# Optimization experiments

Hardware: AMD Instinct MI355X
Metric: run time of the kernel (lower is better)

Reference implementation:

```python
import jax, jax.numpy as jnp
import numpy as np
import math

B, S, T, D, H = 4, 1024, 1024, 512, 8
EPS = 1e-5

def setup_inputs() -> dict:
    key = jax.random.key(0)
    ks = iter(jax.random.split(key, 40))
    w = lambda *shp: jax.random.normal(next(ks), shp, jnp.float32) * 0.02
    inp = {
        'x': jax.random.normal(next(ks), (B, S, D), jnp.float32),
        'encod_out': jax.random.normal(next(ks), (B, T, D), jnp.float32),
    }
    for p in ('sa', 'ca'):
        inp[p + '_wq'] = w(H, D, D); inp[p + '_bq'] = w(H, D)
        inp[p + '_wk'] = w(H, D, D); inp[p + '_bk'] = w(H, D)
        inp[p + '_wv'] = w(H, D, D); inp[p + '_bv'] = w(H, D)
        inp[p + '_wo'] = w(H, D, D); inp[p + '_bo'] = w(H, D)
        inp[p + '_wf'] = w(H * D, D); inp[p + '_bf'] = w(D)
    for i in (1, 2, 3):
        inp[f'ln{i}_g'] = jnp.ones((D,), jnp.float32)
        inp[f'ln{i}_b'] = jnp.zeros((D,), jnp.float32)
    inp['fc1_w'] = w(D, 4 * D); inp['fc1_b'] = w(4 * D)
    inp['fc2_w'] = w(4 * D, D); inp['fc2_b'] = w(D)
    return inp

def _ln(x, g, b):
    m = jnp.mean(x, -1, keepdims=True)
    v = jnp.mean((x - m) ** 2, -1, keepdims=True)
    return (x - m) / jnp.sqrt(v + EPS) * g + b

def _mha(xq, xkv, wq, bq, wk, bk, wv, bv, wo, bo, wf, bf, mask):
    # per-head FULL-width projections, stacked on head axis h
    Q = jnp.einsum('bsd,hdf->bhsf', xq, wq) + bq[None, :, None, :]
    K = jnp.einsum('btd,hdf->bhtf', xkv, wk) + bk[None, :, None, :]
    V = jnp.einsum('btd,hdf->bhtf', xkv, wv) + bv[None, :, None, :]
    scores = jnp.einsum('bhsf,bhtf->bhst', Q, K) / math.sqrt(Q.shape[-1])
    if mask is not None:
        scores = jnp.where(mask == 0, -jnp.inf, scores)
    A = jax.nn.softmax(scores, axis=-1)
    O = jnp.einsum('bhst,bhtf->bhsf', A, V)
    O = jnp.einsum('bhsf,hfg->bhsg', O, wo) + bo[None, :, None, :]  # per-head out_linear
    cat = O.transpose(0, 2, 1, 3).reshape(O.shape[0], O.shape[2], -1)  # [B,S,H*D]
    return cat @ wf + bf

def reference(x, encod_out,
              sa_wq, sa_bq, sa_wk, sa_bk, sa_wv, sa_bv, sa_wo, sa_bo, sa_wf, sa_bf,
              ca_wq, ca_bq, ca_wk, ca_bk, ca_wv, ca_bv, ca_wo, ca_bo, ca_wf, ca_bf,
              ln1_g, ln1_b, ln2_g, ln2_b, ln3_g, ln3_b,
              fc1_w, fc1_b, fc2_w, fc2_b):
    s = x.shape[1]
    mask = jnp.tril(jnp.ones((s, s), x.dtype))
    h = _mha(x, x, sa_wq, sa_bq, sa_wk, sa_bk, sa_wv, sa_bv, sa_wo, sa_bo, sa_wf, sa_bf, mask)
    x1 = _ln(h + x, ln1_g, ln1_b)
    h = _mha(x1, encod_out, ca_wq, ca_bq, ca_wk, ca_bk, ca_wv, ca_bv, ca_wo, ca_bo, ca_wf, ca_bf, None)
    x2 = _ln(h + x1, ln2_g, ln2_b)
    ff = jax.nn.relu(x2 @ fc1_w + fc1_b) @ fc2_w + fc2_b
    return _ln(ff + x2, ln3_g, ln3_b)
```

## Files before the change

kernel.cpp:

```cpp
#include <hip/hip_runtime.h>
#include <hip/hip_bf16.h>

typedef __hip_bfloat16 bf16;
typedef __attribute__((ext_vector_type(8))) __bf16 bf16x8;
typedef __attribute__((ext_vector_type(4))) float f32x4;

typedef const __attribute__((address_space(1))) void cg_void;
typedef __attribute__((address_space(3))) void lds_void;

__device__ inline float b2f(bf16 v) { return __bfloat162float(v); }
__device__ inline bf16 f2b(float v) { return __float2bfloat16(v); }
__device__ inline float ldf(const float* p) { return *p; }
__device__ inline float ldf(const bf16* p) { return __bfloat162float(*p); }

#define BKK 32

template<int BN_, bool BIAS, bool RELU, bool OUT_BF16>
__global__ __launch_bounds__(256) void gemm_bt(
    const bf16* __restrict__ A, const bf16* __restrict__ Bt, void* __restrict__ Cout,
    const float* __restrict__ bias,
    int M, int N, int K, int lda, int ldb, int ldc,
    long aHi, long aLo, long bHi, long bLo, long cHi, long cLo, int zdiv)
{
  alignas(16) __shared__ bf16 As[128 * BKK];
  alignas(16) __shared__ bf16 Bs[BN_ * BKK];
  const int t = threadIdx.x;
  const int l = t & 63;
  const int w = t >> 6;
  const int z = blockIdx.z;
  const int zq = z / zdiv, zr = z % zdiv;
  A += (long)zq * aHi + (long)zr * aLo;
  Bt += (long)zq * bHi + (long)zr * bLo;
  const long cbase = (long)zq * cHi + (long)zr * cLo;

  const int gx = gridDim.x;
  int bid = blockIdx.y * gx + blockIdx.x;
  const int nwg = gx * gridDim.y;
  if ((nwg & 7) == 0)
    bid = (bid & 7) * (nwg >> 3) + (bid >> 3);
  const int m0 = (bid % gx) * 128;
  const int n0 = (bid / gx) * BN_;

  constexpr int NJ = BN_ / 32;
  f32x4 acc[4][NJ] = {};

  const int r0 = t >> 2;
  const int kc = (t & 3) * 8;
  const bf16* aP0 = A + (long)(m0 + r0) * lda + kc;
  const bf16* aP1 = aP0 + (long)64 * lda;
  bf16* aD0 = As + t * 8;
  bf16* aD1 = As + (t + 256) * 8;
  const bf16* bP0 = Bt + (long)(n0 + r0) * ldb + kc;
  bf16* bD0 = Bs + t * 8;
  const bf16* bP1 = bP0 + (long)64 * ldb;
  bf16* bD1 = Bs + (t + 256) * 8;

  const int fr = l & 15;
  const int fk = (l >> 4) * 8;
  const int aRow = (w >> 1) * 64 + fr;
  const int bRow = (w & 1) * (BN_ / 2) + fr;

  for (int kt = 0; kt < K; kt += BKK) {
    __builtin_amdgcn_global_load_lds((cg_void*)(aP0 + kt), (lds_void*)aD0, 16, 0, 0);
    __builtin_amdgcn_global_load_lds((cg_void*)(aP1 + kt), (lds_void*)aD1, 16, 0, 0);
    __builtin_amdgcn_global_load_lds((cg_void*)(bP0 + kt), (lds_void*)bD0, 16, 0, 0);
    if constexpr (BN_ == 128)
      __builtin_amdgcn_global_load_lds((cg_void*)(bP1 + kt), (lds_void*)bD1, 16, 0, 0);
    __syncthreads();
    bf16x8 af[4], bv[NJ];
#pragma unroll
    for (int i = 0; i < 4; ++i)
      af[i] = *(const bf16x8*)(As + (aRow + i * 16) * BKK + fk);
#pragma unroll
    for (int j = 0; j < NJ; ++j)
      bv[j] = *(const bf16x8*)(Bs + (bRow + j * 16) * BKK + fk);
#pragma unroll
    for (int i = 0; i < 4; ++i)
#pragma unroll
      for (int j = 0; j < NJ; ++j)
        acc[i][j] = __builtin_amdgcn_mfma_f32_16x16x32_bf16(af[i], bv[j], acc[i][j], 0, 0, 0);
    __syncthreads();
  }

  float* cf = (float*)Cout;
  bf16* cb = (bf16*)Cout;
#pragma unroll
  for (int i = 0; i < 4; ++i) {
    const int mb = m0 + (w >> 1) * 64 + i * 16 + ((l >> 4) << 2);
#pragma unroll
    for (int j = 0; j < NJ; ++j) {
      const int nc = n0 + (w & 1) * (BN_ / 2) + j * 16 + fr;
      const float bvv = BIAS ? bias[nc] : 0.f;
#pragma unroll
      for (int r = 0; r < 4; ++r) {
        const int m = mb + r;
        const long off = cbase + (long)m * ldc + nc;
        float vv = acc[i][j][r] + bvv;
        if (RELU) vv = fmaxf(vv, 0.f);
        if (OUT_BF16) cb[off] = f2b(vv);
        else cf[off] = vv;
      }
    }
  }
}

template<int BN_, bool B_, bool R_, bool O_>
static inline void gemmL(hipStream_t st, int M, int N, int K,
                         const bf16* A, int lda, long aHi, long aLo,
                         const bf16* Bt, int ldb, long bHi, long bLo,
                         void* C, int ldc, long cHi, long cLo,
                         int zdiv, int nz, const float* bias)
{
  dim3 g(M / 128, N / BN_, nz);
  gemm_bt<BN_, B_, R_, O_><<<g, dim3(256), 0, st>>>(
      A, Bt, C, bias, M, N, K, lda, ldb, ldc, aHi, aLo, bHi, bLo, cHi, cLo, zdiv);
}

template<typename ST>
__global__ __launch_bounds__(256) void transpose_to_bf16(
    const ST* __restrict__ in, bf16* __restrict__ out, int R, int C, long sIn, long sOut)
{
  __shared__ bf16 tile[32][33];
  const int z = blockIdx.z;
  in += (long)z * sIn;
  out += (long)z * sOut;
  const int tx = threadIdx.x & 31, ty = threadIdx.x >> 5;
  const int c0 = blockIdx.x * 32, r0 = blockIdx.y * 32;
#pragma unroll
  for (int i = 0; i < 4; ++i)
    tile[ty + i * 8][tx] = f2b(ldf(in + (long)(r0 + ty + i * 8) * C + c0 + tx));
  __syncthreads();
#pragma unroll
  for (int i = 0; i < 4; ++i)
    out[(long)(c0 + ty + i * 8) * R + r0 + tx] = tile[tx][ty + i * 8];
}

__global__ __launch_bounds__(256) void cast4_k(
    const float* __restrict__ in, bf16* __restrict__ out, long n4)
{
  long i = (long)blockIdx.x * 256 + threadIdx.x;
  const long st = (long)gridDim.x * 256;
  for (; i < n4; i += st) {
    const float4 v = ((const float4*)in)[i];
    bf16* o = out + i * 4;
    o[0] = f2b(v.x); o[1] = f2b(v.y); o[2] = f2b(v.z); o[3] = f2b(v.w);
  }
}

__global__ __launch_bounds__(256) void cast4x4_k(
    const float* __restrict__ p0, const float* __restrict__ p1,
    const float* __restrict__ p2, const float* __restrict__ p3,
    bf16* __restrict__ o0, bf16* __restrict__ o1,
    bf16* __restrict__ o2, bf16* __restrict__ o3, long n4)
{
  const float* in; bf16* out;
  switch (blockIdx.y) {
    case 0: in = p0; out = o0; break;
    case 1: in = p1; out = o1; break;
    case 2: in = p2; out = o2; break;
    default: in = p3; out = o3; break;
  }
  long i = (long)blockIdx.x * 256 + threadIdx.x;
  const long st = (long)gridDim.x * 256;
  for (; i < n4; i += st) {
    const float4 v = ((const float4*)in)[i];
    bf16* o = out + i * 4;
    o[0] = f2b(v.x); o[1] = f2b(v.y); o[2] = f2b(v.z); o[3] = f2b(v.w);
  }
}

__global__ __launch_bounds__(256) void fill_sentinel(float* __restrict__ out, long n)
{
  long i = (long)blockIdx.x * 256 + threadIdx.x;
  const long st = (long)gridDim.x * 256;
  for (; i < n; i += st) out[i] = 1.0e6f;
}

__global__ __launch_bounds__(256) void softmax_rows(
    bf16* __restrict__ S, const float* __restrict__ v, float scale, int causal)
{
  const int r = blockIdx.x * 4 + (threadIdx.x >> 6);
  const int l = threadIdx.x & 63;
  const int zl = r >> 10, s = r & 1023;
  bf16* row = S + (long)r * 1024;
  const float* vp = v + (zl >> 2) * 4096 + (zl & 3) * 1024;
  const int t0 = l * 16;
  bf16x8* rp = (bf16x8*)(row + t0);
  const bf16x8 a0 = rp[0], a1 = rp[1];
  float xx[16];
#pragma unroll
  for (int j = 0; j < 8; ++j) { xx[j] = (float)a0[j]; xx[8 + j] = (float)a1[j]; }
  float mx = -3.4e38f;
#pragma unroll
  for (int k = 0; k < 16; ++k) {
    const int tt = t0 + k;
    float val = (xx[k] + vp[tt]) * scale;
    if (causal && tt > s) val = -3.4e38f;
    xx[k] = val;
    mx = fmaxf(mx, val);
  }
#pragma unroll
  for (int d = 1; d < 64; d <<= 1) mx = fmaxf(mx, __shfl_xor(mx, d));
  float sum = 0.f;
#pragma unroll
  for (int k = 0; k < 16; ++k) {
    const float e = (xx[k] > -1e37f) ? __expf(xx[k] - mx) : 0.f;
    xx[k] = e;
    sum += e;
  }
#pragma unroll
  for (int d = 1; d < 64; d <<= 1) sum += __shfl_xor(sum, d);
  const float inv = 1.f / sum;
  bf16x8 r0v, r1v;
#pragma unroll
  for (int j = 0; j < 8; ++j) {
    r0v[j] = (__bf16)(xx[j] * inv);
    r1v[j] = (__bf16)(xx[8 + j] * inv);
  }
  rp[0] = r0v;
  rp[1] = r1v;
}

__global__ __launch_bounds__(256) void ln_fused(
    const float* __restrict__ parts, long zstride, int nz,
    const float* __restrict__ beff, const float* __restrict__ resF,
    const bf16* __restrict__ resB, const float* __restrict__ g,
    const float* __restrict__ b, bf16* __restrict__ outB, float* __restrict__ outF)
{
  const int m = blockIdx.x * 4 + (threadIdx.x >> 6);
  const int l = threadIdx.x & 63;
  float vv[8];
  float s = 0.f;
#pragma unroll
  for (int i = 0; i < 8; ++i) {
    const int c = i * 64 + l;
    float acc = beff[c];
    if (resF) acc += resF[(long)m * 512 + c];
    else acc += b2f(resB[(long)m * 512 + c]);
    for (int zz = 0; zz < nz; ++zz) acc += parts[zz * zstride + (long)m * 512 + c];
    vv[i] = acc;
    s += acc;
  }
#pragma unroll
  for (int d = 1; d < 64; d <<= 1) s += __shfl_xor(s, d);
  const float mean = s * (1.f / 512.f);
  float vs = 0.f;
#pragma unroll
  for (int i = 0; i < 8; ++i) { const float dv = vv[i] - mean; vs += dv * dv; }
#pragma unroll
  for (int d = 1; d < 64; d <<= 1) vs += __shfl_xor(vs, d);
  const float rstd = rsqrtf(vs * (1.f / 512.f) + 1e-5f);
#pragma unroll
  for (int i = 0; i < 8; ++i) {
    const int c = i * 64 + l;
    const float y = (vv[i] - mean) * rstd * g[c] + b[c];
    if (outB) outB[(long)m * 512 + c] = f2b(y);
    if (outF) outF[(long)m * 512 + c] = y;
  }
}

__global__ void beff_init_k(const float* __restrict__ bf_, float* __restrict__ beff)
{
  const int e = blockIdx.x * 256 + threadIdx.x;
  if (e < 512) beff[e] = bf_[e];
}

__global__ __launch_bounds__(256) void beff_wf_k(
    const float* __restrict__ bo, const float* __restrict__ wf, float* __restrict__ beff)
{
  const int t = threadIdx.x;
  const int r0 = blockIdx.x * 128;
  float s0 = 0.f, s1 = 0.f;
  for (int r = 0; r < 128; ++r) {
    const float bb = bo[r0 + r];
    const float* row = wf + (long)(r0 + r) * 512;
    s0 += bb * row[t];
    s1 += bb * row[t + 256];
  }
  atomicAdd(&beff[t], s0);
  atomicAdd(&beff[t + 256], s1);
}

__global__ __launch_bounds__(256) void beff_w2_k(
    const float* __restrict__ bv, const bf16* __restrict__ W2t, float* __restrict__ beff)
{
  const int e = blockIdx.x * 4 + (threadIdx.x >> 6);
  const int l = threadIdx.x & 63;
  const bf16* row = W2t + (long)e * 4096;
  float s = 0.f;
#pragma unroll
  for (int j = 0; j < 8; ++j) {
    const int hf = j * 512 + l * 8;
    const bf16x8 wv = *(const bf16x8*)(row + hf);
    const float4 b0 = *(const float4*)(bv + hf);
    const float4 b1 = *(const float4*)(bv + hf + 4);
    s += (float)wv[0] * b0.x + (float)wv[1] * b0.y + (float)wv[2] * b0.z + (float)wv[3] * b0.w;
    s += (float)wv[4] * b1.x + (float)wv[5] * b1.y + (float)wv[6] * b1.z + (float)wv[7] * b1.w;
  }
#pragma unroll
  for (int d = 1; d < 64; d <<= 1) s += __shfl_xor(s, d);
  if (l == 0) atomicAdd(&beff[e], s);
}

__global__ __launch_bounds__(256) void wkbq_k(
    const float* __restrict__ wk, const float* __restrict__ bq, float* __restrict__ o)
{
  const int id = blockIdx.x * 4 + (threadIdx.x >> 6);
  const int l = threadIdx.x & 63;
  const int h = id >> 9, d = id & 511;
  const float* wp = wk + (long)h * 262144 + (long)d * 512 + l * 8;
  const float* bp = bq + h * 512 + l * 8;
  float s = 0.f;
#pragma unroll
  for (int j = 0; j < 2; ++j) {
    const float4 a = *(const float4*)(wp + j * 4);
    const float4 b = *(const float4*)(bp + j * 4);
    s += a.x * b.x + a.y * b.y + a.z * b.z + a.w * b.w;
  }
#pragma unroll
  for (int dd = 1; dd < 64; dd <<= 1) s += __shfl_xor(s, dd);
  if (l == 0) o[id] = s;
}

__global__ __launch_bounds__(256) void rank1_v(
    const bf16* __restrict__ kvB, const float* __restrict__ wkbq, float* __restrict__ v)
{
  const int m = blockIdx.x * 4 + (threadIdx.x >> 6);
  const int l = threadIdx.x & 63;
  const bf16x8 row = *(const bf16x8*)(kvB + (long)m * 512 + l * 8);
  float rf[8];
#pragma unroll
  for (int j = 0; j < 8; ++j) rf[j] = (float)row[j];
  for (int h = 0; h < 8; ++h) {
    const float* wp = wkbq + h * 512 + l * 8;
    float p = 0.f;
#pragma unroll
    for (int j = 0; j < 8; ++j) p += rf[j] * wp[j];
#pragma unroll
    for (int d = 1; d < 64; d <<= 1) p += __shfl_xor(p, d);
    if (l == 0) v[(long)h * 4096 + m] = p;
  }
}

extern "C" void kernel_launch(void* const* d_in, const int* in_sizes, int n_in,
                              void* d_out, int out_size, void* d_ws, size_t ws_size,
                              hipStream_t stream)
{
  (void)in_sizes; (void)n_in;
  const float* x = (const float*)d_in[0];
  const float* enc = (const float*)d_in[1];
  const float* ln_g[3] = {(const float*)d_in[22], (const float*)d_in[24], (const float*)d_in[26]};
  const float* ln_b[3] = {(const float*)d_in[23], (const float*)d_in[25], (const float*)d_in[27]};
  const float* fc1_w = (const float*)d_in[28];
  const float* fc1_b = (const float*)d_in[29];
  const float* fc2_w = (const float*)d_in[30];
  const float* fc2_b = (const float*)d_in[31];

  const float scale = 0.044194173824159216f;
  char* base = (char*)d_ws;
  const long MB = 1024 * 1024;

  bf16* Xb    = (bf16*)(base + 0 * MB);
  bf16* Eb    = (bf16*)(base + 4 * MB);
  bf16* x1b   = (bf16*)(base + 8 * MB);
  bf16* x2b   = (bf16*)(base + 12 * MB);
  bf16* fc1T  = (bf16*)(base + 16 * MB);
  bf16* fc2T  = (bf16*)(base + 18 * MB);
  float* vbuf = (float*)(base + 20 * MB);
  float* wkbq = (float*)(base + 20 * MB + 256 * 1024);
  float* beff = (float*)(base + 20 * MB + 512 * 1024);
  bf16* XT    = (bf16*)(base + 21 * MB);
  bf16* WqkT  = (bf16*)(base + 25 * MB);
  bf16* W3cat = (bf16*)(base + 29 * MB);
  bf16* T     = (bf16*)(base + 33 * MB);
  float* parts = (float*)(base + 65 * MB);
  bf16* scores = (bf16*)(base + 97 * MB);
  bf16* AX    = (bf16*)(base + 161 * MB);
  bf16* wqB   = (bf16*)(base + 97 * MB);
  bf16* wkB   = (bf16*)(base + 101 * MB);
  bf16* wvB   = (bf16*)(base + 105 * MB);
  bf16* woB   = (bf16*)(base + 109 * MB);
  bf16* wfT   = (bf16*)(base + 113 * MB);
  bf16* W2t   = (bf16*)(base + 117 * MB);
  bf16* Hb    = (bf16*)(base + 97 * MB);

  if (ws_size < (size_t)(193 * MB)) {
    fill_sentinel<<<dim3(2048), dim3(256), 0, stream>>>((float*)d_out, (long)out_size);
    return;
  }

  cast4_k<<<dim3(512), dim3(256), 0, stream>>>(x, Xb, 4096L * 512 / 4);
  cast4_k<<<dim3(512), dim3(256), 0, stream>>>(enc, Eb, 4096L * 512 / 4);
  transpose_to_bf16<float><<<dim3(64, 16, 1), dim3(256), 0, stream>>>(fc1_w, fc1T, 512, 2048, 0, 0);
  transpose_to_bf16<float><<<dim3(16, 64, 1), dim3(256), 0, stream>>>(fc2_w, fc2T, 2048, 512, 0, 0);

  auto run_attn = [&](int ib, const bf16* qB, const bf16* kvB,
                      const float* resF, const bf16* resB, int causal,
                      const float* lg, const float* lb, bf16* outB) {
    const float* wq = (const float*)d_in[ib + 0];
    const float* bq = (const float*)d_in[ib + 1];
    const float* wk = (const float*)d_in[ib + 2];
    const float* wv = (const float*)d_in[ib + 4];
    const float* bv = (const float*)d_in[ib + 5];
    const float* wo = (const float*)d_in[ib + 6];
    const float* bo = (const float*)d_in[ib + 7];
    const float* wf = (const float*)d_in[ib + 8];
    const float* bfv = (const float*)d_in[ib + 9];

    cast4x4_k<<<dim3(512, 4), dim3(256), 0, stream>>>(
        wq, wk, wv, wo, wqB, wkB, wvB, woB, 2097152 / 4);
    transpose_to_bf16<float><<<dim3(16, 128, 1), dim3(256), 0, stream>>>(wf, wfT, 4096, 512, 0, 0);
    gemmL<64, false, false, true>(stream, 512, 512, 512,
        wfT, 4096, 512, 0, woB, 512, 262144, 0, W2t, 4096, 512, 0, 1, 8, nullptr);
    beff_init_k<<<dim3(2), dim3(256), 0, stream>>>(bfv, beff);
    beff_wf_k<<<dim3(32), dim3(256), 0, stream>>>(bo, wf, beff);
    beff_w2_k<<<dim3(128), dim3(256), 0, stream>>>(bv, W2t, beff);
    gemmL<64, false, false, true>(stream, 512, 512, 512,
        wkB, 512, 262144, 0, wqB, 512, 262144, 0, WqkT, 512, 262144, 0, 1, 8, nullptr);
    gemmL<64, false, false, true>(stream, 512, 512, 512,
        W2t, 4096, 512, 0, wvB, 512, 262144, 0, W3cat, 4096, 512, 0, 1, 8, nullptr);
    wkbq_k<<<dim3(1024), dim3(256), 0, stream>>>(wk, bq, wkbq);
    rank1_v<<<dim3(1024), dim3(256), 0, stream>>>(kvB, wkbq, vbuf);
    transpose_to_bf16<bf16><<<dim3(16, 32, 4), dim3(256), 0, stream>>>(
        kvB, XT, 1024, 512, 524288, 524288);
    gemmL<128, false, false, true>(stream, 4096, 4096, 512,
        qB, 512, 0, 0, WqkT, 512, 0, 0, T, 4096, 0, 0, 1, 1, nullptr);

    gemmL<128, false, false, true>(stream, 1024, 1024, 512,
        T, 4096, 512, 4194304,
        kvB, 512, 0, 524288,
        scores, 1024, 4194304, 1048576, 4, 32, nullptr);
    softmax_rows<<<dim3(8192), dim3(256), 0, stream>>>(scores, vbuf, scale, causal);
    gemmL<64, false, false, true>(stream, 1024, 512, 1024,
        scores, 1024, 4194304, 1048576,
        XT, 1024, 0, 524288,
        AX, 4096, 512, 4194304, 4, 32, nullptr);
    gemmL<64, false, false, false>(stream, 4096, 512, 1024,
        AX, 4096, 1024, 0, W3cat, 4096, 1024, 0,
        parts, 512, 2097152, 0, 1, 4, nullptr);
    ln_fused<<<dim3(1024), dim3(256), 0, stream>>>(
        parts, 2097152, 4, beff, resF, resB, lg, lb, outB, nullptr);
  };

  run_attn(2, Xb, Xb, x, nullptr, 1, ln_g[0], ln_b[0], x1b);
  run_attn(12, x1b, Eb, nullptr, x1b, 0, ln_g[1], ln_b[1], x2b);

  gemmL<128, true, true, true>(stream, 4096, 2048, 512,
      x2b, 512, 0, 0, fc1T, 512, 0, 0, Hb, 2048, 0, 0, 1, 1, fc1_b);
  gemmL<64, false, false, false>(stream, 4096, 512, 512,
      Hb, 2048, 512, 0, fc2T, 2048, 512, 0, parts, 512, 2097152, 0, 1, 4, nullptr);
  ln_fused<<<dim3(1024), dim3(256), 0, stream>>>(
      parts, 2097152, 4, fc2_b, nullptr, x2b, ln_g[2], ln_b[2], nullptr, (float*)d_out);
}
```

Baseline: 959.2 us.

## Triple-buffer GEMM LDS tiles with async prefetch two stages ahead

Turns the bf16 GEMM main loop into a three-stage software pipeline. Tiles are fetched with global_load_lds two iterations ahead, and manual vmcnt waits plus raw barriers replace the per-iteration __syncthreads pair. It also extends the workgroup swizzle to cover the z (batch/head) dimension. The goal is to hide global memory latency behind MFMA work, at the cost of three times the LDS use (which may lower occupancy). It also depends on hand-counted vmcnt values that must match the number of loads issued.

```diff
diff --git a/kernel.cpp b/kernel.cpp
--- a/kernel.cpp
+++ b/kernel.cpp
@@ -14,6 +14,12 @@
 __device__ inline float ldf(const bf16* p) { return __bfloat162float(*p); }
 
 #define BKK 32
+
+template<int N> __device__ __forceinline__ void wait_vm() {
+  if constexpr (N == 0) asm volatile("s_waitcnt vmcnt(0)" ::: "memory");
+  else if constexpr (N == 3) asm volatile("s_waitcnt vmcnt(3)" ::: "memory");
+  else asm volatile("s_waitcnt vmcnt(4)" ::: "memory");
+}
 
 template<int BN_, bool BIAS, bool RELU, bool OUT_BF16>
 __global__ __launch_bounds__(256) void gemm_bt(
@@ -22,25 +28,28 @@
     int M, int N, int K, int lda, int ldb, int ldc,
     long aHi, long aLo, long bHi, long bLo, long cHi, long cLo, int zdiv)
 {
-  alignas(16) __shared__ bf16 As[128 * BKK];
-  alignas(16) __shared__ bf16 Bs[BN_ * BKK];
+  constexpr int NL = (BN_ == 128) ? 4 : 3;
+  alignas(16) __shared__ bf16 As[3][128 * BKK];
+  alignas(16) __shared__ bf16 Bs[3][BN_ * BKK];
   const int t = threadIdx.x;
   const int l = t & 63;
   const int w = t >> 6;
-  const int z = blockIdx.z;
+
+  const int gx = gridDim.x;
+  const long gxy = (long)gx * gridDim.y;
+  long flat = (long)blockIdx.z * gxy + (long)blockIdx.y * gx + blockIdx.x;
+  const long total = gxy * gridDim.z;
+  if ((total & 7) == 0) flat = (flat & 7) * (total >> 3) + (flat >> 3);
+  const int z = (int)(flat / gxy);
+  const int rem = (int)(flat % gxy);
+  const int m0 = (rem % gx) * 128;
+  const int n0 = (rem / gx) * BN_;
+
   const int zq = z / zdiv, zr = z % zdiv;
   A += (long)zq * aHi + (long)zr * aLo;
   Bt += (long)zq * bHi + (long)zr * bLo;
   const long cbase = (long)zq * cHi + (long)zr * cLo;
 
-  const int gx = gridDim.x;
-  int bid = blockIdx.y * gx + blockIdx.x;
-  const int nwg = gx * gridDim.y;
-  if ((nwg & 7) == 0)
-    bid = (bid & 7) * (nwg >> 3) + (bid >> 3);
-  const int m0 = (bid % gx) * 128;
-  const int n0 = (bid / gx) * BN_;
-
   constexpr int NJ = BN_ / 32;
   f32x4 acc[4][NJ] = {};
 
@@ -48,38 +57,51 @@
   const int kc = (t & 3) * 8;
   const bf16* aP0 = A + (long)(m0 + r0) * lda + kc;
   const bf16* aP1 = aP0 + (long)64 * lda;
-  bf16* aD0 = As + t * 8;
-  bf16* aD1 = As + (t + 256) * 8;
   const bf16* bP0 = Bt + (long)(n0 + r0) * ldb + kc;
-  bf16* bD0 = Bs + t * 8;
   const bf16* bP1 = bP0 + (long)64 * ldb;
-  bf16* bD1 = Bs + (t + 256) * 8;
 
   const int fr = l & 15;
   const int fk = (l >> 4) * 8;
   const int aRow = (w >> 1) * 64 + fr;
   const int bRow = (w & 1) * (BN_ / 2) + fr;
 
-  for (int kt = 0; kt < K; kt += BKK) {
-    __builtin_amdgcn_global_load_lds((cg_void*)(aP0 + kt), (lds_void*)aD0, 16, 0, 0);
-    __builtin_amdgcn_global_load_lds((cg_void*)(aP1 + kt), (lds_void*)aD1, 16, 0, 0);
-    __builtin_amdgcn_global_load_lds((cg_void*)(bP0 + kt), (lds_void*)bD0, 16, 0, 0);
+  const int nt = K >> 5;
+
+  auto stage = [&](int tt, int bi) {
+    const long kt = (long)tt * BKK;
+    __builtin_amdgcn_global_load_lds((cg_void*)(aP0 + kt), (lds_void*)(&As[bi][t * 8]), 16, 0, 0);
+    __builtin_amdgcn_global_load_lds((cg_void*)(aP1 + kt), (lds_void*)(&As[bi][(t + 256) * 8]), 16, 0, 0);
+    __builtin_amdgcn_global_load_lds((cg_void*)(bP0 + kt), (lds_void*)(&Bs[bi][t * 8]), 16, 0, 0);
     if constexpr (BN_ == 128)
-      __builtin_amdgcn_global_load_lds((cg_void*)(bP1 + kt), (lds_void*)bD1, 16, 0, 0);
-    __syncthreads();
+      __builtin_amdgcn_global_load_lds((cg_void*)(bP1 + kt), (lds_void*)(&Bs[bi][(t + 256) * 8]), 16, 0, 0);
+  };
+
+  stage(0, 0);
+  stage(1, 1);
+  wait_vm<NL>();
+  __builtin_amdgcn_s_barrier();
+
+  int bi = 0;
+  for (int tt = 0; tt < nt; ++tt) {
+    if (tt + 2 < nt) stage(tt + 2, bi == 0 ? 2 : bi - 1);
     bf16x8 af[4], bv[NJ];
 #pragma unroll
     for (int i = 0; i < 4; ++i)
-      af[i] = *(const bf16x8*)(As + (aRow + i * 16) * BKK + fk);
+      af[i] = *(const bf16x8*)(&As[bi][(aRow + i * 16) * BKK + fk]);
 #pragma unroll
     for (int j = 0; j < NJ; ++j)
-      bv[j] = *(const bf16x8*)(Bs + (bRow + j * 16) * BKK + fk);
+      bv[j] = *(const bf16x8*)(&Bs[bi][(bRow + j * 16) * BKK + fk]);
 #pragma unroll
     for (int i = 0; i < 4; ++i)
 #pragma unroll
       for (int j = 0; j < NJ; ++j)
         acc[i][j] = __builtin_amdgcn_mfma_f32_16x16x32_bf16(af[i], bv[j], acc[i][j], 0, 0, 0);
-    __syncthreads();
+    if (tt + 1 < nt) {
+      if (tt + 2 < nt) wait_vm<NL>();
+      else wait_vm<0>();
+      __builtin_amdgcn_s_barrier();
+    }
+    bi = (bi == 2) ? 0 : bi + 1;
   }
 
   float* cf = (float*)Cout;
```

Measured after the change: 797.2 us. 1.2x faster.
